# Kernel optimization log

Hardware: AMD Instinct MI355X
Metric: run time of the kernel (lower is better)

Reference implementation:

```python
import jax, jax.numpy as jnp
import numpy as np
from jax import lax

B, C, H, W = 32, 3, 128, 128
S = 10             # max_segments
L = 200            # base_traj_length
TOTAL_LIMIT = 200  # traj_length (must equal L per original sample())
DOF = 2
HID = 2048
CONV_OUT = 512 * 6 * 6  # 128->126->63->61->30->28->14->12->6


def _conv(x, w, b):
    y = lax.conv_general_dilated(x, w, (1, 1), 'VALID', dimension_numbers=('NCHW', 'OIHW', 'NCHW'))
    return y + b[None, :, None, None]


def _pool_relu(x):
    return jax.nn.relu(lax.reduce_window(x, -jnp.inf, lax.max, (1, 1, 2, 2), (1, 1, 2, 2), 'VALID'))


def _rotate2d(y, y0, rot):
    # rotate points y (B,L,2) around per-batch center y0 (B,2) by rot (B,1,1) radians
    px, py = y[..., 0:1], y[..., 1:2]
    cx, cy = y0[:, 0][:, None, None], y0[:, 1][:, None, None]
    c, s = jnp.cos(rot), jnp.sin(rot)
    return jnp.concatenate([c * (px - cx) - s * (py - cy) + cx,
                            s * (px - cx) + c * (py - cy) + cy], axis=2)


def _sample(traj, ratio):
    b, T = traj.shape[0], traj.shape[1]
    f32 = traj.dtype
    seg_limit = jnp.ceil(ratio * TOTAL_LIMIT)  # (B,S)
    # redistribution: shave 1 off the (first) max segment while over budget.
    # original runs over_limit.max() iterations; over_limit <= S-1, extras are no-ops (still_over gate).
    for _ in range(S):
        max_val = seg_limit.max(axis=1)
        still_over = (seg_limit.sum(axis=1) != float(L)).astype(f32)
        reduced = jnp.ones((b,), f32)
        for j in range(S):
            mult = jnp.abs(jnp.sign(max_val - seg_limit[:, j]) - 1.0)
            seg_limit = seg_limit.at[:, j].add(-mult * reduced * still_over)
            reduced = jnp.clip(reduced - mult, 0.0)
    seg_ids = np.arange(T) // L
    # replicates original condition: i>0 and cur_segment_idx != floor(i - 1/L)  (note: i - 1/L, as written)
    forces = np.array([(i > 0) and (seg_ids[i] != int(np.floor(i - 1.0 / L))) for i in range(T)])
    di0 = jnp.floor((L - 1.0) / seg_limit[:, 0:1])
    init = (di0, jnp.zeros((b, 1), f32), jnp.zeros((b, 1), f32), jnp.zeros((b, S), f32))

    def step(state, inp):
        di, last_idx, n_tot, seg_cnt = state
        i_f, seg, force = inp
        lim = lax.dynamic_index_in_dim(seg_limit, seg, axis=1, keepdims=True)  # (B,1)
        cnt = lax.dynamic_index_in_dim(seg_cnt, seg, axis=1, keepdims=True)    # (B,1)
        new_di = jnp.floor((L - 1.0 - (last_idx - seg.astype(f32) * L)) / (lim - cnt))
        di = jnp.where(force | (di < new_di), new_di, di)
        chk = (jnp.sign(jnp.clip(TOTAL_LIMIT - n_tot, 0.0))
               * (cnt < lim).astype(f32)
               * (i_f - last_idx == di).astype(f32))
        last_idx = jnp.maximum(last_idx, i_f * chk)
        seg_cnt = lax.dynamic_update_index_in_dim(seg_cnt, (cnt + chk)[:, 0], seg, axis=1)
        return (di, last_idx, n_tot + chk, seg_cnt), chk[:, 0]

    xs = (jnp.arange(T, dtype=f32), jnp.asarray(seg_ids, jnp.int32), jnp.asarray(forces))
    _, mask_t = lax.scan(step, init, xs)
    mask = mask_t.T > 0  # (B,T) velocity mask; exactly TOTAL_LIMIT true per row
    idx = jnp.argsort(jnp.where(mask, 0, 1), axis=1)[:, :TOTAL_LIMIT]  # stable sort -> ordered true positions
    return jnp.take_along_axis(traj, idx[:, :, None], axis=1)


def _forward(x, w1, b1, w2, b2, w3, b3, w4, b4, fcw1, fcb1, fcw2, fcb2,
             wi, bi, ws, bs, wr, br, base_traj):
    h = _pool_relu(_conv(x, w1, b1))
    h = _pool_relu(_conv(h, w2, b2))
    h = _pool_relu(_conv(h, w3, b3))
    h = _pool_relu(_conv(h, w4, b4))
    feat = h.reshape(h.shape[0], -1)  # (B, CONV_OUT)
    z = jnp.tanh(feat @ fcw1.T + fcb1)
    z = z @ fcw2.T + fcb2             # dropout == identity (eval mode)
    init_pos = z @ wi.T + bi                                   # (B,DOF)
    seg_mod = (z @ ws.T + bs).reshape(z.shape[0], S, DOF + 1)  # (B,S,DOF+1)
    ratio = jax.nn.softmax(z @ wr.T + br, axis=1)              # (B,S)
    last_pos = init_pos[:, None, :]
    starts, segs = [last_pos], []
    for i in range(S):
        scaling = seg_mod[:, i, :-1]
        rot = jnp.tanh(seg_mod[:, i, -1])[:, None, None] * 3.14
        m = base_traj * scaling[:, None, :]
        m = _rotate2d(m, m[:, 0, :], rot)
        m = last_pos + m
        last_pos = m[:, -1:, :]
        starts.append(last_pos)
        segs.append(m)
    traj = jnp.concatenate(segs, axis=1)             # (B,S*L,DOF) unsampled
    seg_start_end = jnp.concatenate(starts, axis=1)  # (B,S+1,DOF)
    sampled = _sample(traj, ratio)                   # (B,TOTAL_LIMIT,DOF)
    return sampled, seg_start_end, ratio, traj


def setup_inputs():
    key = jax.random.key(0)
    ks = jax.random.split(key, 12)
    n = lambda k, s, sc: jax.random.normal(k, s, jnp.float32) * sc
    t = jnp.linspace(0.0, 1.0, L)
    base_traj = jnp.stack([t, jnp.sin(t * jnp.pi)], axis=-1)[None]  # (1,L,2)
    return {
        'x': n(ks[0], (B, C, H, W), 1.0),
        'w1': n(ks[1], (64, C, 3, 3), 0.05), 'b1': jnp.zeros((64,), jnp.float32),
        'w2': n(ks[2], (128, 64, 3, 3), 0.05), 'b2': jnp.zeros((128,), jnp.float32),
        'w3': n(ks[3], (256, 128, 3, 3), 0.05), 'b3': jnp.zeros((256,), jnp.float32),
        'w4': n(ks[4], (512, 256, 3, 3), 0.05), 'b4': jnp.zeros((512,), jnp.float32),
        'fcw1': n(ks[5], (HID, CONV_OUT), 0.01), 'fcb1': jnp.zeros((HID,), jnp.float32),
        'fcw2': n(ks[6], (HID, HID), 0.02), 'fcb2': jnp.zeros((HID,), jnp.float32),
        'wi': n(ks[7], (DOF, HID), 0.02), 'bi': jnp.zeros((DOF,), jnp.float32),
        'ws': n(ks[8], (S * (DOF + 1), HID), 0.02), 'bs': jnp.zeros((S * (DOF + 1),), jnp.float32),
        'wr': n(ks[9], (S, HID), 0.05), 'br': jnp.zeros((S,), jnp.float32),
        'base_traj': base_traj,
    }


def reference(x, w1, b1, w2, b2, w3, b3, w4, b4, fcw1, fcb1, fcw2, fcb2,
              wi, bi, ws, bs, wr, br, base_traj):
    return _forward(x, w1, b1, w2, b2, w3, b3, w4, b4, fcw1, fcb1, fcw2, fcb2,
                    wi, bi, ws, bs, wr, br, base_traj)
```

## Files before the change

### kernel.cpp

```cpp
#include <hip/hip_runtime.h>

__global__ __launch_bounds__(256)
void conv1_lds(const float* __restrict__ in, const float* __restrict__ wt,
               const float* __restrict__ bias, float* __restrict__ out)
{
    __shared__ float sh[3][34][34];
    int bx = blockIdx.x;
    int tile = bx & 15;
    int cg   = (bx >> 4) & 7;
    int b    = bx >> 7;
    int tr = tile >> 2, tc = tile & 3;
    int tid = threadIdx.x;
    int ty = tid >> 4, tx = tid & 15;
    int R0 = 32 * tr, C0 = 32 * tc;

    for (int t = tid; t < 3 * 34 * 34; t += 256) {
        int ci = t / 1156;
        int rem = t - ci * 1156;
        int rr = rem / 34, cc = rem - rr * 34;
        int gr = R0 + rr; if (gr > 127) gr = 127;
        int gc = C0 + cc; if (gc > 127) gc = 127;
        sh[ci][rr][cc] = in[(((size_t)b * 3 + ci) * 128 + gr) * 128 + gc];
    }
    __syncthreads();

    float acc[8][2][2] = {};
    int co0 = cg * 8;
#pragma unroll
    for (int ci = 0; ci < 3; ++ci) {
        float p[4][4];
#pragma unroll
        for (int r = 0; r < 4; ++r) {
            const float2* pr = reinterpret_cast<const float2*>(&sh[ci][2 * ty + r][2 * tx]);
            float2 a = pr[0], c2 = pr[1];
            p[r][0] = a.x; p[r][1] = a.y; p[r][2] = c2.x; p[r][3] = c2.y;
        }
#pragma unroll
        for (int j = 0; j < 8; ++j) {
            const float* wj = wt + ((size_t)(co0 + j) * 3 + ci) * 9;
#pragma unroll
            for (int kh = 0; kh < 3; ++kh)
#pragma unroll
                for (int kw = 0; kw < 3; ++kw) {
                    float wv = wj[kh * 3 + kw];
#pragma unroll
                    for (int dy = 0; dy < 2; ++dy)
#pragma unroll
                        for (int dx = 0; dx < 2; ++dx)
                            acc[j][dy][dx] = fmaf(wv, p[dy + kh][dx + kw], acc[j][dy][dx]);
                }
        }
    }
    int py = 16 * tr + ty, px = 16 * tc + tx;
    if (py < 63 && px < 63) {
#pragma unroll
        for (int j = 0; j < 8; ++j) {
            float v = fmaxf(fmaxf(acc[j][0][0], acc[j][0][1]),
                            fmaxf(acc[j][1][0], acc[j][1][1])) + bias[co0 + j];
            out[(((size_t)b * 64 + co0 + j) * 63 + py) * 63 + px] = fmaxf(v, 0.f);
        }
    }
}

__global__ __launch_bounds__(256)
void conv2_db(const float* __restrict__ in, const float* __restrict__ wt,
              const float* __restrict__ bias, float* __restrict__ out)
{
    __shared__ __align__(16) float sh[4][32][34];

    int bx = blockIdx.x;
    int tile = bx & 3;
    int cg   = (bx >> 2) & 15;
    int b    = bx >> 6;
    int thi = tile >> 1, twi = tile & 1;
    int R0 = 30 * thi, C0 = 30 * twi;

    int tid = threadIdx.x;
    int ty = tid / 15, tx = tid - ty * 15;
    bool active = (tid < 225);
    int co0 = cg * 8;

    float acc[8][2][2] = {};
    float sr[16];

#pragma unroll
    for (int j = 0; j < 16; ++j) {
        int t = tid + 256 * j;
        int ci = t >> 10;
        int rem = t & 1023;
        int rr = rem >> 5, cc = rem & 31;
        sr[j] = in[(((size_t)b * 64 + ci) * 63 + (R0 + rr)) * 63 + (C0 + cc)];
    }

    for (int it = 0; it < 16; ++it) {
#pragma unroll
        for (int j = 0; j < 16; ++j) {
            int t = tid + 256 * j;
            int ci = t >> 10;
            int rem = t & 1023;
            int rr = rem >> 5, cc = rem & 31;
            sh[ci][rr][cc] = sr[j];
        }
        __syncthreads();
        if (it < 15) {
            int ci0n = (it + 1) * 4;
#pragma unroll
            for (int j = 0; j < 16; ++j) {
                int t = tid + 256 * j;
                int ci = t >> 10;
                int rem = t & 1023;
                int rr = rem >> 5, cc = rem & 31;
                sr[j] = in[(((size_t)b * 64 + ci0n + ci) * 63 + (R0 + rr)) * 63 + (C0 + cc)];
            }
        }
        if (active) {
            int ci0 = it * 4;
#pragma unroll
            for (int ci = 0; ci < 4; ++ci) {
                float p[4][4];
#pragma unroll
                for (int r = 0; r < 4; ++r) {
                    const float2* pr = reinterpret_cast<const float2*>(&sh[ci][2 * ty + r][2 * tx]);
                    float2 a = pr[0], c2 = pr[1];
                    p[r][0] = a.x; p[r][1] = a.y; p[r][2] = c2.x; p[r][3] = c2.y;
                }
#pragma unroll
                for (int j = 0; j < 8; ++j) {
                    const float* wj = wt + ((size_t)(co0 + j) * 64 + (ci0 + ci)) * 9;
#pragma unroll
                    for (int kh = 0; kh < 3; ++kh)
#pragma unroll
                        for (int kw = 0; kw < 3; ++kw) {
                            float wv = wj[kh * 3 + kw];
#pragma unroll
                            for (int dy = 0; dy < 2; ++dy)
#pragma unroll
                                for (int dx = 0; dx < 2; ++dx)
                                    acc[j][dy][dx] = fmaf(wv, p[dy + kh][dx + kw], acc[j][dy][dx]);
                        }
                }
            }
        }
        __syncthreads();
    }
    if (active) {
        int py = 15 * thi + ty, px = 15 * twi + tx;
#pragma unroll
        for (int j = 0; j < 8; ++j) {
            float v = fmaxf(fmaxf(acc[j][0][0], acc[j][0][1]),
                            fmaxf(acc[j][1][0], acc[j][1][1])) + bias[co0 + j];
            out[(((size_t)b * 128 + co0 + j) * 30 + py) * 30 + px] = fmaxf(v, 0.f);
        }
    }
}

__global__ __launch_bounds__(256)
void conv3_db(const float* __restrict__ in, const float* __restrict__ wt,
              const float* __restrict__ bias, float* __restrict__ out)
{
    __shared__ float4 sh4[900];
    float* shf = reinterpret_cast<float*>(sh4);

    int bx = blockIdx.x;
    int cg = bx & 31;
    int b  = bx >> 5;
    int tid = threadIdx.x;
    int ty = tid / 14, tx = tid - ty * 14;
    bool active = (tid < 196);
    int co0 = cg * 8;

    float acc[8][2][2] = {};
    float4 sr[4];

    const float4* gp0 = reinterpret_cast<const float4*>(in + (size_t)b * 128 * 900);
#pragma unroll
    for (int j = 0; j < 4; ++j) {
        int idx = tid + 256 * j;
        if (idx < 900) sr[j] = gp0[idx];
    }

    for (int it = 0; it < 32; ++it) {
#pragma unroll
        for (int j = 0; j < 4; ++j) {
            int idx = tid + 256 * j;
            if (idx < 900) sh4[idx] = sr[j];
        }
        __syncthreads();
        if (it < 31) {
            const float4* gpn = gp0 + (size_t)(it + 1) * 900;
#pragma unroll
            for (int j = 0; j < 4; ++j) {
                int idx = tid + 256 * j;
                if (idx < 900) sr[j] = gpn[idx];
            }
        }
        if (active) {
            int ci0 = it * 4;
#pragma unroll
            for (int ci = 0; ci < 4; ++ci) {
                const float* base = shf + ci * 900;
                float p[4][4];
#pragma unroll
                for (int r = 0; r < 4; ++r) {
                    const float2* pr = reinterpret_cast<const float2*>(base + (2 * ty + r) * 30 + 2 * tx);
                    float2 a = pr[0], c2 = pr[1];
                    p[r][0] = a.x; p[r][1] = a.y; p[r][2] = c2.x; p[r][3] = c2.y;
                }
#pragma unroll
                for (int j = 0; j < 8; ++j) {
                    const float* wj = wt + ((size_t)(co0 + j) * 128 + (ci0 + ci)) * 9;
#pragma unroll
                    for (int kh = 0; kh < 3; ++kh)
#pragma unroll
                        for (int kw = 0; kw < 3; ++kw) {
                            float wv = wj[kh * 3 + kw];
#pragma unroll
                            for (int dy = 0; dy < 2; ++dy)
#pragma unroll
                                for (int dx = 0; dx < 2; ++dx)
                                    acc[j][dy][dx] = fmaf(wv, p[dy + kh][dx + kw], acc[j][dy][dx]);
                        }
                }
            }
        }
        __syncthreads();
    }
    if (active) {
#pragma unroll
        for (int j = 0; j < 8; ++j) {
            float v = fmaxf(fmaxf(acc[j][0][0], acc[j][0][1]),
                            fmaxf(acc[j][1][0], acc[j][1][1])) + bias[co0 + j];
            out[(((size_t)b * 256 + co0 + j) * 14 + ty) * 14 + tx] = fmaxf(v, 0.f);
        }
    }
}

__global__ __launch_bounds__(256)
void conv4_v3(const float* __restrict__ in, const float* __restrict__ wt,
              const float* __restrict__ bias, float* __restrict__ out)
{
    __shared__ __align__(16) float smem[4032 + 4 * 16 * 37];
    float* in_sh = smem;
    float* w_sh  = smem + 4032;
    float* red   = smem;

    int bx = blockIdx.x;
    int cg = bx & 31;
    int b  = bx >> 5;
    int tid = threadIdx.x;
    int h   = tid >> 6;
    int r6  = tid & 63;
    int cog = r6 >> 3;
    int sub = r6 & 7;
    int R = 3 * (sub >> 1), C = 6 * (sub & 1);

    float acc[2][3][6] = {};
    float sin_r[13];
    float sw_r[9];

    const size_t in_b = (size_t)b * 256 * 196;

#pragma unroll
    for (int j = 0; j < 13; ++j) {
        int g = tid + 256 * j;
        if (g < 3136) {
            int hh = g / 784, rem = g - hh * 784;
            int ci = rem / 196, r2 = rem - ci * 196;
            sin_r[j] = in[in_b + (size_t)(hh * 64 + ci) * 196 + r2];
        }
    }
#pragma unroll
    for (int j = 0; j < 9; ++j) {
        int g = tid + 256 * j;
        int hh = g / 576, rem = g - hh * 576;
        int co = rem / 36, q = rem - co * 36;
        sw_r[j] = wt[(size_t)(cg * 16 + co) * 2304 + (size_t)(hh * 64) * 9 + q];
    }

    for (int it = 0; it < 16; ++it) {
#pragma unroll
        for (int j = 0; j < 13; ++j) {
            int g = tid + 256 * j;
            if (g < 3136) {
                int hh = g / 784, rem = g - hh * 784;
                int ci = rem / 196, r2 = rem - ci * 196;
                int rr = r2 / 14, cc = r2 - rr * 14;
                in_sh[((hh * 4 + ci) * 14 + rr) * 18 + cc] = sin_r[j];
            }
        }
#pragma unroll
        for (int j = 0; j < 9; ++j) {
            int g = tid + 256 * j;
            int hh = g / 576, rem = g - hh * 576;
            int co = rem / 36, q = rem - co * 36;
            w_sh[(hh * 16 + co) * 37 + q] = sw_r[j];
        }
        __syncthreads();
        if (it < 15) {
            int k0n = (it + 1) * 4;
#pragma unroll
            for (int j = 0; j < 13; ++j) {
                int g = tid + 256 * j;
                if (g < 3136) {
                    int hh = g / 784, rem = g - hh * 784;
                    int ci = rem / 196, r2 = rem - ci * 196;
                    sin_r[j] = in[in_b + (size_t)(hh * 64 + k0n + ci) * 196 + r2];
                }
            }
#pragma unroll
            for (int j = 0; j < 9; ++j) {
                int g = tid + 256 * j;
                int hh = g / 576, rem = g - hh * 576;
                int co = rem / 36, q = rem - co * 36;
                sw_r[j] = wt[(size_t)(cg * 16 + co) * 2304 + (size_t)(hh * 64 + k0n) * 9 + q];
            }
        }
#pragma unroll
        for (int ci = 0; ci < 4; ++ci) {
            float w[2][9];
#pragma unroll
            for (int c = 0; c < 2; ++c)
#pragma unroll
                for (int k = 0; k < 9; ++k)
                    w[c][k] = w_sh[(h * 16 + 2 * cog + c) * 37 + ci * 9 + k];
            const float* rowbase = in_sh + ((h * 4 + ci) * 14) * 18;
#pragma unroll
            for (int r = 0; r < 5; ++r) {
                float row[8];
                const float2* pr = reinterpret_cast<const float2*>(rowbase + (size_t)(R + r) * 18 + C);
                float2 a0 = pr[0], a1 = pr[1], a2 = pr[2], a3 = pr[3];
                row[0] = a0.x; row[1] = a0.y; row[2] = a1.x; row[3] = a1.y;
                row[4] = a2.x; row[5] = a2.y; row[6] = a3.x; row[7] = a3.y;
#pragma unroll
                for (int y = 0; y < 3; ++y) {
                    if (y < r - 2 || y > r) continue;
                    int kh = r - y;
#pragma unroll
                    for (int c = 0; c < 2; ++c)
#pragma unroll
                        for (int kw = 0; kw < 3; ++kw) {
                            float wv = w[c][kh * 3 + kw];
#pragma unroll
                            for (int x = 0; x < 6; ++x)
                                acc[c][y][x] = fmaf(wv, row[x + kw], acc[c][y][x]);
                        }
                }
            }
        }
        __syncthreads();
    }
#pragma unroll
    for (int hh = 0; hh < 4; ++hh) {
        if (h == hh) {
#pragma unroll
            for (int c = 0; c < 2; ++c)
#pragma unroll
                for (int y = 0; y < 3; ++y)
#pragma unroll
                    for (int x = 0; x < 6; ++x) {
                        float* dst = &red[((2 * cog + c) * 12 + R + y) * 13 + C + x];
                        if (hh == 0) *dst = acc[c][y][x];
                        else         *dst += acc[c][y][x];
                    }
        }
        __syncthreads();
    }
    for (int t = tid; t < 576; t += 256) {
        int co = t / 36, rem = t - co * 36;
        int pr = rem / 6, pc = rem - pr * 6;
        const float* rp = &red[(co * 12 + 2 * pr) * 13 + 2 * pc];
        float v = fmaxf(fmaxf(rp[0], rp[1]), fmaxf(rp[13], rp[14]));
        v += bias[cg * 16 + co];
        out[(((size_t)b * 512 + cg * 16 + co) * 6 + pr) * 6 + pc] = fmaxf(v, 0.f);
    }
}

__global__ __launch_bounds__(1024)
void fc_big(const float* __restrict__ X, const float* __restrict__ W,
            const float* __restrict__ bias, float* __restrict__ Y,
            int K, int N, int act)
{
    __shared__ float red[32][32][8];
    int o0 = blockIdx.x * 8;
    int s = threadIdx.x & 31;
    int b = threadIdx.x >> 5;
    int K4 = K >> 2;
    const float4* X4 = reinterpret_cast<const float4*>(X) + (size_t)b * K4;
    const float4* W4 = reinterpret_cast<const float4*>(W);

    float acc[8] = {};
    for (int k4 = s; k4 < K4; k4 += 32) {
        float4 xv = X4[k4];
#pragma unroll
        for (int o = 0; o < 8; ++o) {
            float4 wv = W4[(size_t)(o0 + o) * K4 + k4];
            acc[o] = fmaf(xv.x, wv.x,
                     fmaf(xv.y, wv.y,
                     fmaf(xv.z, wv.z,
                     fmaf(xv.w, wv.w, acc[o]))));
        }
    }
#pragma unroll
    for (int o = 0; o < 8; ++o) red[b][s][o] = acc[o];
    __syncthreads();
    if (threadIdx.x < 256) {
        int bb = threadIdx.x >> 3, oo = threadIdx.x & 7;
        float v = bias[o0 + oo];
#pragma unroll 8
        for (int ss = 0; ss < 32; ++ss) v += red[bb][ss][oo];
        if (act) v = tanhf(v);
        Y[(size_t)bb * N + o0 + oo] = v;
    }
}

__global__ __launch_bounds__(256)
void fc_two(const float* __restrict__ X, const float* __restrict__ W,
            const float* __restrict__ bias, float* __restrict__ Y,
            int K, int N, int act)
{
    int o0 = blockIdx.x * 2;
    int tid = threadIdx.x;
    const float* w0 = W + (size_t)o0 * K;
    const float* w1 = w0 + K;
    float a0[32], a1[32];
#pragma unroll
    for (int b = 0; b < 32; ++b) { a0[b] = 0.f; a1[b] = 0.f; }

    for (int k = tid; k < K; k += 256) {
        float wv0 = w0[k], wv1 = w1[k];
#pragma unroll
        for (int b = 0; b < 32; ++b) {
            float xv = X[(size_t)b * K + k];
            a0[b] = fmaf(wv0, xv, a0[b]);
            a1[b] = fmaf(wv1, xv, a1[b]);
        }
    }
    __shared__ float part[2][4][32];
    int lane = tid & 63, wv = tid >> 6;
#pragma unroll
    for (int b = 0; b < 32; ++b) {
        float s0 = a0[b], s1 = a1[b];
#pragma unroll
        for (int off = 32; off >= 1; off >>= 1) {
            s0 += __shfl_down(s0, off);
            s1 += __shfl_down(s1, off);
        }
        if (lane == 0) { part[0][wv][b] = s0; part[1][wv][b] = s1; }
    }
    __syncthreads();
    if (tid < 64) {
        int j = tid >> 5, b = tid & 31;
        float s = part[j][0][b] + part[j][1][b] + part[j][2][b] + part[j][3][b] + bias[o0 + j];
        if (act) s = tanhf(s);
        Y[(size_t)b * N + o0 + j] = s;
    }
}

__global__ __launch_bounds__(64)
void post_kernel(const float* __restrict__ logits, float* __restrict__ ratio_out,
                 float* __restrict__ sl_out)
{
    int b = threadIdx.x;
    if (b >= 32) return;
    float lg[10];
#pragma unroll
    for (int j = 0; j < 10; ++j) lg[j] = logits[b * 10 + j];
    float mx = lg[0];
#pragma unroll
    for (int j = 1; j < 10; ++j) mx = fmaxf(mx, lg[j]);
    float e[10]; float ssum = 0.f;
#pragma unroll
    for (int j = 0; j < 10; ++j) { e[j] = expf(lg[j] - mx); ssum += e[j]; }
    float sl[10];
#pragma unroll
    for (int j = 0; j < 10; ++j) {
        float r = e[j] / ssum;
        ratio_out[b * 10 + j] = r;
        sl[j] = ceilf(r * 200.f);
    }
#pragma unroll
    for (int it = 0; it < 10; ++it) {
        float s = 0.f, mx2 = sl[0];
#pragma unroll
        for (int j = 0; j < 10; ++j) { s += sl[j]; mx2 = fmaxf(mx2, sl[j]); }
        float over = (s != 200.f) ? 1.f : 0.f;
        float reduced = 1.f;
#pragma unroll
        for (int j = 0; j < 10; ++j) {
            float mult = (sl[j] == mx2) ? 1.f : 0.f;
            sl[j] -= mult * reduced * over;
            reduced = fmaxf(reduced - mult, 0.f);
        }
    }
#pragma unroll
    for (int j = 0; j < 10; ++j) sl_out[b * 10 + j] = sl[j];
}

__global__ __launch_bounds__(256)
void traj_kernel(const float* __restrict__ base, const float* __restrict__ ipos,
                 const float* __restrict__ sm, float* __restrict__ out_traj,
                 float* __restrict__ out_starts)
{
    int b = blockIdx.x;
    int j = threadIdx.x;
    float bx0 = base[0], by0 = base[1];
    float bxL = base[398], byL = base[399];
    float bx = 0.f, by = 0.f;
    if (j < 200) { bx = base[2 * j]; by = base[2 * j + 1]; }
    float curx = ipos[b * 2 + 0], cury = ipos[b * 2 + 1];
    if (j == 0) { out_starts[b * 22 + 0] = curx; out_starts[b * 22 + 1] = cury; }
#pragma unroll
    for (int i = 0; i < 10; ++i) {
        float sx  = sm[b * 30 + i * 3 + 0];
        float sy  = sm[b * 30 + i * 3 + 1];
        float rot = tanhf(sm[b * 30 + i * 3 + 2]) * 3.14f;
        float c = cosf(rot), s = sinf(rot);
        float cx = bx0 * sx, cy = by0 * sy;
        if (j < 200) {
            float px = bx * sx, py = by * sy;
            float rx = c * (px - cx) - s * (py - cy) + cx;
            float ry = s * (px - cx) + c * (py - cy) + cy;
            size_t o = ((size_t)b * 2000 + i * 200 + j) * 2;
            out_traj[o + 0] = curx + rx;
            out_traj[o + 1] = cury + ry;
        }
        float pxL = bxL * sx, pyL = byL * sy;
        float exL = c * (pxL - cx) - s * (pyL - cy) + cx;
        float eyL = s * (pxL - cx) + c * (pyL - cy) + cy;
        curx += exL; cury += eyL;
        if (j == 0) {
            out_starts[b * 22 + (i + 1) * 2 + 0] = curx;
            out_starts[b * 22 + (i + 1) * 2 + 1] = cury;
        }
    }
}

__global__ __launch_bounds__(64)
void sample_kernel(const float* __restrict__ sl_in, const float* __restrict__ traj,
                   float* __restrict__ samp_out)
{
    __shared__ unsigned int maskb[32][63];
    __shared__ float ssl[32][10];
    int tid = threadIdx.x;
    for (int t = tid; t < 32 * 63; t += 64) ((unsigned int*)maskb)[t] = 0u;
    for (int t = tid; t < 32 * 10; t += 64) ((float*)ssl)[t] = sl_in[t];
    __syncthreads();
    if (tid >= 32) return;
    int b = tid;
    const float* tb = traj + (size_t)b * 4000;
    float* sp = samp_out + (size_t)b * 400;
    int out_n = 0;
    float last = 0.f, ntot = 0.f;
    float lim0 = ssl[b][0];
    float di = floorf(199.f / lim0);
    float ct0 = 0.f;
    if ((ntot < 200.f) && (ct0 < lim0) && (0.f - last == di)) {
        ntot += 1.f; ct0 += 1.f;
        maskb[b][0] |= 1u;
        sp[out_n * 2] = tb[0]; sp[out_n * 2 + 1] = tb[1]; ++out_n;
    }
    {
        float ndi = floorf((199.f - last) / (lim0 - ct0));
        if (di < ndi) di = ndi;
        if ((ntot < 200.f) && (ct0 < lim0) && (1.f - last == di)) {
            last = 1.f; ntot += 1.f; ct0 += 1.f;
            maskb[b][0] |= 2u;
            sp[out_n * 2] = tb[2]; sp[out_n * 2 + 1] = tb[3]; ++out_n;
        }
    }
    for (int seg = 0; seg < 10; ++seg) {
        float lim = ssl[b][seg];
        float ct = (seg == 0) ? ct0 : 0.f;
        float segbase = 200.f * seg;
        float segend = segbase + 199.f;
        float pos = (seg == 0) ? 2.f : segbase;
        float ndi = floorf((199.f - (last - segbase)) / (lim - ct));
        while ((ntot < 200.f) && (ct < lim)) {
            float fi = last + ndi;
            if (!(fi >= pos && fi <= segend)) break;
            int i = (int)fi;
            last = fi; ntot += 1.f; ct += 1.f;
            maskb[b][i >> 5] |= (1u << (i & 31));
            sp[out_n * 2] = tb[2 * i]; sp[out_n * 2 + 1] = tb[2 * i + 1]; ++out_n;
            pos = fi + 1.f;
            ndi = floorf((199.f - (last - segbase)) / (lim - ct));
        }
    }
    for (int i = 0; i < 2000 && out_n < 200; ++i) {
        if (!((maskb[b][i >> 5] >> (i & 31)) & 1u)) {
            sp[out_n * 2] = tb[2 * i]; sp[out_n * 2 + 1] = tb[2 * i + 1]; ++out_n;
        }
    }
}

extern "C" void kernel_launch(void* const* d_in, const int* in_sizes, int n_in,
                              void* d_out, int out_size, void* d_ws, size_t ws_size,
                              hipStream_t stream)
{
    const float* x    = (const float*)d_in[0];
    const float* w1   = (const float*)d_in[1];
    const float* b1   = (const float*)d_in[2];
    const float* w2   = (const float*)d_in[3];
    const float* b2   = (const float*)d_in[4];
    const float* w3   = (const float*)d_in[5];
    const float* b3   = (const float*)d_in[6];
    const float* w4   = (const float*)d_in[7];
    const float* b4   = (const float*)d_in[8];
    const float* fcw1 = (const float*)d_in[9];
    const float* fcb1 = (const float*)d_in[10];
    const float* fcw2 = (const float*)d_in[11];
    const float* fcb2 = (const float*)d_in[12];
    const float* wi   = (const float*)d_in[13];
    const float* bi   = (const float*)d_in[14];
    const float* wsw  = (const float*)d_in[15];
    const float* bs   = (const float*)d_in[16];
    const float* wr   = (const float*)d_in[17];
    const float* br   = (const float*)d_in[18];
    const float* base = (const float*)d_in[19];

    float* out = (float*)d_out;
    float* ws  = (float*)d_ws;

    float* p1   = ws + 0;
    float* p2   = ws + 8128512;
    float* p3   = ws + 0;
    float* feat = ws + 8128512;
    float* z1   = ws + 0;
    float* z2   = ws + 65536;
    float* ipos = ws + 131072;
    float* smod = ws + 131136;
    float* rlog = ws + 132096;
    float* slim = ws + 132416;

    float* out_samp   = out;
    float* out_starts = out + 12800;
    float* out_ratio  = out + 13504;
    float* out_traj   = out + 13824;

    conv1_lds<<<4096, 256, 0, stream>>>(x, w1, b1, p1);
    conv2_db<<<2048, 256, 0, stream>>>(p1, w2, b2, p2);
    conv3_db<<<1024, 256, 0, stream>>>(p2, w3, b3, p3);
    conv4_v3<<<1024, 256, 0, stream>>>(p3, w4, b4, feat);

    fc_big<<<256, 1024, 0, stream>>>(feat, fcw1, fcb1, z1, 18432, 2048, 1);
    fc_big<<<256, 1024, 0, stream>>>(z1, fcw2, fcb2, z2, 2048, 2048, 0);

    fc_two<<<1, 256, 0, stream>>>(z2, wi, bi, ipos, 2048, 2, 0);
    fc_two<<<15, 256, 0, stream>>>(z2, wsw, bs, smod, 2048, 30, 0);
    fc_two<<<5, 256, 0, stream>>>(z2, wr, br, rlog, 2048, 10, 0);

    post_kernel<<<1, 64, 0, stream>>>(rlog, out_ratio, slim);
    traj_kernel<<<32, 256, 0, stream>>>(base, ipos, smod, out_traj, out_starts);
    sample_kernel<<<1, 64, 0, stream>>>(slim, out_traj, out_samp);
}
```

Baseline: 994.9 us.

## Double-buffer LDS in conv2/conv3 and widen conv2 to 16 output channels

Conv2 and conv3 now keep two shared-memory input buffers, so each iteration needs one barrier instead of two, and the next chunk is written to the spare buffer after compute. Conv2 also computes 16 output channels per block instead of 8, which halves the grid and the redundant input tile loads per channel. The cost is more registers (64 accumulators in conv2) and twice the shared memory, which may reduce occupancy.

Measured after the change: 1.206 ms. 21.3% more time.

```diff
diff --git a/kernel.cpp b/kernel.cpp
--- a/kernel.cpp
+++ b/kernel.cpp
@@ -63,24 +63,24 @@
 }
 
 __global__ __launch_bounds__(256)
-void conv2_db(const float* __restrict__ in, const float* __restrict__ wt,
+void conv2_v3(const float* __restrict__ in, const float* __restrict__ wt,
               const float* __restrict__ bias, float* __restrict__ out)
 {
-    __shared__ __align__(16) float sh[4][32][34];
+    __shared__ __align__(16) float sh[2][4][32][34];
 
     int bx = blockIdx.x;
     int tile = bx & 3;
-    int cg   = (bx >> 2) & 15;
-    int b    = bx >> 6;
+    int cg   = (bx >> 2) & 7;
+    int b    = bx >> 5;
     int thi = tile >> 1, twi = tile & 1;
     int R0 = 30 * thi, C0 = 30 * twi;
 
     int tid = threadIdx.x;
     int ty = tid / 15, tx = tid - ty * 15;
     bool active = (tid < 225);
-    int co0 = cg * 8;
-
-    float acc[8][2][2] = {};
+    int co0 = cg * 16;
+
+    float acc[16][2][2] = {};
     float sr[16];
 
 #pragma unroll
@@ -91,17 +91,18 @@
         int rr = rem >> 5, cc = rem & 31;
         sr[j] = in[(((size_t)b * 64 + ci) * 63 + (R0 + rr)) * 63 + (C0 + cc)];
     }
+#pragma unroll
+    for (int j = 0; j < 16; ++j) {
+        int t = tid + 256 * j;
+        int ci = t >> 10;
+        int rem = t & 1023;
+        int rr = rem >> 5, cc = rem & 31;
+        sh[0][ci][rr][cc] = sr[j];
+    }
+    __syncthreads();
 
     for (int it = 0; it < 16; ++it) {
-#pragma unroll
-        for (int j = 0; j < 16; ++j) {
-            int t = tid + 256 * j;
-            int ci = t >> 10;
-            int rem = t & 1023;
-            int rr = rem >> 5, cc = rem & 31;
-            sh[ci][rr][cc] = sr[j];
-        }
-        __syncthreads();
+        int cur = it & 1;
         if (it < 15) {
             int ci0n = (it + 1) * 4;
 #pragma unroll
@@ -114,19 +115,18 @@
             }
         }
         if (active) {
-            int ci0 = it * 4;
 #pragma unroll
             for (int ci = 0; ci < 4; ++ci) {
                 float p[4][4];
 #pragma unroll
                 for (int r = 0; r < 4; ++r) {
-                    const float2* pr = reinterpret_cast<const float2*>(&sh[ci][2 * ty + r][2 * tx]);
+                    const float2* pr = reinterpret_cast<const float2*>(&sh[cur][ci][2 * ty + r][2 * tx]);
                     float2 a = pr[0], c2 = pr[1];
                     p[r][0] = a.x; p[r][1] = a.y; p[r][2] = c2.x; p[r][3] = c2.y;
                 }
 #pragma unroll
-                for (int j = 0; j < 8; ++j) {
-                    const float* wj = wt + ((size_t)(co0 + j) * 64 + (ci0 + ci)) * 9;
+                for (int j = 0; j < 16; ++j) {
+                    const float* wj = wt + ((size_t)(co0 + j) * 64 + (it * 4 + ci)) * 9;
 #pragma unroll
                     for (int kh = 0; kh < 3; ++kh)
 #pragma unroll
@@ -141,12 +141,22 @@
                 }
             }
         }
+        if (it < 15) {
+#pragma unroll
+            for (int j = 0; j < 16; ++j) {
+                int t = tid + 256 * j;
+                int ci = t >> 10;
+                int rem = t & 1023;
+                int rr = rem >> 5, cc = rem & 31;
+                sh[cur ^ 1][ci][rr][cc] = sr[j];
+            }
+        }
         __syncthreads();
     }
     if (active) {
         int py = 15 * thi + ty, px = 15 * twi + tx;
 #pragma unroll
-        for (int j = 0; j < 8; ++j) {
+        for (int j = 0; j < 16; ++j) {
             float v = fmaxf(fmaxf(acc[j][0][0], acc[j][0][1]),
                             fmaxf(acc[j][1][0], acc[j][1][1])) + bias[co0 + j];
             out[(((size_t)b * 128 + co0 + j) * 30 + py) * 30 + px] = fmaxf(v, 0.f);
@@ -158,8 +168,7 @@
 void conv3_db(const float* __restrict__ in, const float* __restrict__ wt,
               const float* __restrict__ bias, float* __restrict__ out)
 {
-    __shared__ float4 sh4[900];
-    float* shf = reinterpret_cast<float*>(sh4);
+    __shared__ float4 sh4[2][900];
 
     int bx = blockIdx.x;
     int cg = bx & 31;
@@ -178,14 +187,15 @@
         int idx = tid + 256 * j;
         if (idx < 900) sr[j] = gp0[idx];
     }
+#pragma unroll
+    for (int j = 0; j < 4; ++j) {
+        int idx = tid + 256 * j;
+        if (idx < 900) sh4[0][idx] = sr[j];
+    }
+    __syncthreads();
 
     for (int it = 0; it < 32; ++it) {
-#pragma unroll
-        for (int j = 0; j < 4; ++j) {
-            int idx = tid + 256 * j;
-            if (idx < 900) sh4[idx] = sr[j];
-        }
-        __syncthreads();
+        int cur = it & 1;
         if (it < 31) {
             const float4* gpn = gp0 + (size_t)(it + 1) * 900;
 #pragma unroll
@@ -195,7 +205,7 @@
             }
         }
         if (active) {
-            int ci0 = it * 4;
+            const float* shf = reinterpret_cast<const float*>(sh4[cur]);
 #pragma unroll
             for (int ci = 0; ci < 4; ++ci) {
                 const float* base = shf + ci * 900;
@@ -208,7 +218,7 @@
                 }
 #pragma unroll
                 for (int j = 0; j < 8; ++j) {
-                    const float* wj = wt + ((size_t)(co0 + j) * 128 + (ci0 + ci)) * 9;
+                    const float* wj = wt + ((size_t)(co0 + j) * 128 + (it * 4 + ci)) * 9;
 #pragma unroll
                     for (int kh = 0; kh < 3; ++kh)
 #pragma unroll
@@ -221,6 +231,13 @@
                                     acc[j][dy][dx] = fmaf(wv, p[dy + kh][dx + kw], acc[j][dy][dx]);
                         }
                 }
+            }
+        }
+        if (it < 31) {
+#pragma unroll
+            for (int j = 0; j < 4; ++j) {
+                int idx = tid + 256 * j;
+                if (idx < 900) sh4[cur ^ 1][idx] = sr[j];
             }
         }
         __syncthreads();
@@ -638,7 +655,7 @@
     float* out_traj   = out + 13824;
 
     conv1_lds<<<4096, 256, 0, stream>>>(x, w1, b1, p1);
-    conv2_db<<<2048, 256, 0, stream>>>(p1, w2, b2, p2);
+    conv2_v3<<<1024, 256, 0, stream>>>(p1, w2, b2, p2);
     conv3_db<<<1024, 256, 0, stream>>>(p2, w3, b3, p3);
     conv4_v3<<<1024, 256, 0, stream>>>(p3, w4, b4, feat);
 
```

## Replace conv2/conv3 with templated register-tiled conv using per-thread channel and 4x8 outputs

Applied to the files above, without the earlier changes.

Conv2 and conv3 are replaced by a single templated kernel. Each thread owns one output channel and a 4x8 pre-pool output patch. Weights are loaded once per input channel into registers and reused across 32 outputs, and the input rows are read from LDS once per row. The old kernels had each thread handle 8 channels and a 2x2 patch, which reloaded weights for every channel and re-read the input. The new layout raises arithmetic intensity and also fixes the thread mapping so all 256 threads do work. The cost is more registers and edge tiles that do wasted compute.

Result: no change. 995.5 us (+0.1%).

```diff
diff --git a/kernel.cpp b/kernel.cpp
--- a/kernel.cpp
+++ b/kernel.cpp
@@ -62,175 +62,115 @@
     }
 }
 
+template<int CIN, int DIM, int POOL, int COUT, int TILES_R, int TILES_C>
 __global__ __launch_bounds__(256)
-void conv2_db(const float* __restrict__ in, const float* __restrict__ wt,
-              const float* __restrict__ bias, float* __restrict__ out)
-{
-    __shared__ __align__(16) float sh[4][32][34];
+void conv_v4(const float* __restrict__ in, const float* __restrict__ wt,
+             const float* __restrict__ bias, float* __restrict__ out)
+{
+    __shared__ __align__(16) float sh[4][18][34];
 
     int bx = blockIdx.x;
-    int tile = bx & 3;
-    int cg   = (bx >> 2) & 15;
-    int b    = bx >> 6;
-    int thi = tile >> 1, twi = tile & 1;
-    int R0 = 30 * thi, C0 = 30 * twi;
-
+    constexpr int NT = TILES_R * TILES_C;
+    constexpr int NCG = COUT / 16;
+    int tile = bx % NT;
+    int cg   = (bx / NT) % NCG;
+    int b    = bx / (NT * NCG);
+    int rt = tile / TILES_C, ct = tile % TILES_C;
     int tid = threadIdx.x;
-    int ty = tid / 15, tx = tid - ty * 15;
-    bool active = (tid < 225);
-    int co0 = cg * 8;
-
-    float acc[8][2][2] = {};
-    float sr[16];
-
-#pragma unroll
-    for (int j = 0; j < 16; ++j) {
+    int co_l = tid & 15;
+    int sp   = tid >> 4;
+    int ty = sp >> 2, tx = sp & 3;
+    int co = cg * 16 + co_l;
+
+    int R0 = 16 * rt, C0 = 32 * ct;
+
+    float acc[4][8] = {};
+    float sr[10];
+
+    const size_t in_b = (size_t)b * CIN * DIM * DIM;
+    const float* wco = wt + (size_t)co * CIN * 9;
+
+#pragma unroll
+    for (int j = 0; j < 10; ++j) {
         int t = tid + 256 * j;
-        int ci = t >> 10;
-        int rem = t & 1023;
-        int rr = rem >> 5, cc = rem & 31;
-        sr[j] = in[(((size_t)b * 64 + ci) * 63 + (R0 + rr)) * 63 + (C0 + cc)];
-    }
-
-    for (int it = 0; it < 16; ++it) {
-#pragma unroll
-        for (int j = 0; j < 16; ++j) {
+        if (t < 2448) {
+            int ci = t / 612;
+            int rem = t - ci * 612;
+            int rr = rem / 34, cc = rem - rr * 34;
+            int gr = R0 + rr; if (gr > DIM - 1) gr = DIM - 1;
+            int gc = C0 + cc; if (gc > DIM - 1) gc = DIM - 1;
+            sr[j] = in[in_b + (size_t)ci * DIM * DIM + gr * DIM + gc];
+        }
+    }
+
+    constexpr int ITERS = CIN / 4;
+    for (int it = 0; it < ITERS; ++it) {
+#pragma unroll
+        for (int j = 0; j < 10; ++j) {
             int t = tid + 256 * j;
-            int ci = t >> 10;
-            int rem = t & 1023;
-            int rr = rem >> 5, cc = rem & 31;
-            sh[ci][rr][cc] = sr[j];
+            if (t < 2448) {
+                int ci = t / 612;
+                int rem = t - ci * 612;
+                int rr = rem / 34, cc = rem - rr * 34;
+                sh[ci][rr][cc] = sr[j];
+            }
         }
         __syncthreads();
-        if (it < 15) {
+        if (it < ITERS - 1) {
             int ci0n = (it + 1) * 4;
 #pragma unroll
-            for (int j = 0; j < 16; ++j) {
+            for (int j = 0; j < 10; ++j) {
                 int t = tid + 256 * j;
-                int ci = t >> 10;
-                int rem = t & 1023;
-                int rr = rem >> 5, cc = rem & 31;
-                sr[j] = in[(((size_t)b * 64 + ci0n + ci) * 63 + (R0 + rr)) * 63 + (C0 + cc)];
-            }
-        }
-        if (active) {
-            int ci0 = it * 4;
-#pragma unroll
-            for (int ci = 0; ci < 4; ++ci) {
-                float p[4][4];
-#pragma unroll
-                for (int r = 0; r < 4; ++r) {
-                    const float2* pr = reinterpret_cast<const float2*>(&sh[ci][2 * ty + r][2 * tx]);
-                    float2 a = pr[0], c2 = pr[1];
-                    p[r][0] = a.x; p[r][1] = a.y; p[r][2] = c2.x; p[r][3] = c2.y;
+                if (t < 2448) {
+                    int ci = t / 612;
+                    int rem = t - ci * 612;
+                    int rr = rem / 34, cc = rem - rr * 34;
+                    int gr = R0 + rr; if (gr > DIM - 1) gr = DIM - 1;
+                    int gc = C0 + cc; if (gc > DIM - 1) gc = DIM - 1;
+                    sr[j] = in[in_b + (size_t)(ci0n + ci) * DIM * DIM + gr * DIM + gc];
                 }
-#pragma unroll
-                for (int j = 0; j < 8; ++j) {
-                    const float* wj = wt + ((size_t)(co0 + j) * 64 + (ci0 + ci)) * 9;
-#pragma unroll
-                    for (int kh = 0; kh < 3; ++kh)
-#pragma unroll
-                        for (int kw = 0; kw < 3; ++kw) {
-                            float wv = wj[kh * 3 + kw];
-#pragma unroll
-                            for (int dy = 0; dy < 2; ++dy)
-#pragma unroll
-                                for (int dx = 0; dx < 2; ++dx)
-                                    acc[j][dy][dx] = fmaf(wv, p[dy + kh][dx + kw], acc[j][dy][dx]);
-                        }
+            }
+        }
+#pragma unroll
+        for (int ci = 0; ci < 4; ++ci) {
+            float w[9];
+#pragma unroll
+            for (int k = 0; k < 9; ++k) w[k] = wco[(it * 4 + ci) * 9 + k];
+#pragma unroll
+            for (int r = 0; r < 6; ++r) {
+                float row[10];
+                const float2* pr = reinterpret_cast<const float2*>(&sh[ci][4 * ty + r][8 * tx]);
+                float2 v0 = pr[0], v1 = pr[1], v2 = pr[2], v3 = pr[3], v4 = pr[4];
+                row[0] = v0.x; row[1] = v0.y; row[2] = v1.x; row[3] = v1.y; row[4] = v2.x;
+                row[5] = v2.y; row[6] = v3.x; row[7] = v3.y; row[8] = v4.x; row[9] = v4.y;
+#pragma unroll
+                for (int y = 0; y < 4; ++y) {
+                    if (y < r - 2 || y > r) continue;
+                    int kh = r - y;
+#pragma unroll
+                    for (int kw = 0; kw < 3; ++kw) {
+                        float wv = w[kh * 3 + kw];
+#pragma unroll
+                        for (int x = 0; x < 8; ++x)
+                            acc[y][x] = fmaf(wv, row[x + kw], acc[y][x]);
+                    }
                 }
             }
         }
         __syncthreads();
     }
-    if (active) {
-        int py = 15 * thi + ty, px = 15 * twi + tx;
-#pragma unroll
-        for (int j = 0; j < 8; ++j) {
-            float v = fmaxf(fmaxf(acc[j][0][0], acc[j][0][1]),
-                            fmaxf(acc[j][1][0], acc[j][1][1])) + bias[co0 + j];
-            out[(((size_t)b * 128 + co0 + j) * 30 + py) * 30 + px] = fmaxf(v, 0.f);
-        }
-    }
-}
-
-__global__ __launch_bounds__(256)
-void conv3_db(const float* __restrict__ in, const float* __restrict__ wt,
-              const float* __restrict__ bias, float* __restrict__ out)
-{
-    __shared__ float4 sh4[900];
-    float* shf = reinterpret_cast<float*>(sh4);
-
-    int bx = blockIdx.x;
-    int cg = bx & 31;
-    int b  = bx >> 5;
-    int tid = threadIdx.x;
-    int ty = tid / 14, tx = tid - ty * 14;
-    bool active = (tid < 196);
-    int co0 = cg * 8;
-
-    float acc[8][2][2] = {};
-    float4 sr[4];
-
-    const float4* gp0 = reinterpret_cast<const float4*>(in + (size_t)b * 128 * 900);
-#pragma unroll
-    for (int j = 0; j < 4; ++j) {
-        int idx = tid + 256 * j;
-        if (idx < 900) sr[j] = gp0[idx];
-    }
-
-    for (int it = 0; it < 32; ++it) {
-#pragma unroll
-        for (int j = 0; j < 4; ++j) {
-            int idx = tid + 256 * j;
-            if (idx < 900) sh4[idx] = sr[j];
-        }
-        __syncthreads();
-        if (it < 31) {
-            const float4* gpn = gp0 + (size_t)(it + 1) * 900;
-#pragma unroll
-            for (int j = 0; j < 4; ++j) {
-                int idx = tid + 256 * j;
-                if (idx < 900) sr[j] = gpn[idx];
-            }
-        }
-        if (active) {
-            int ci0 = it * 4;
-#pragma unroll
-            for (int ci = 0; ci < 4; ++ci) {
-                const float* base = shf + ci * 900;
-                float p[4][4];
-#pragma unroll
-                for (int r = 0; r < 4; ++r) {
-                    const float2* pr = reinterpret_cast<const float2*>(base + (2 * ty + r) * 30 + 2 * tx);
-                    float2 a = pr[0], c2 = pr[1];
-                    p[r][0] = a.x; p[r][1] = a.y; p[r][2] = c2.x; p[r][3] = c2.y;
-                }
-#pragma unroll
-                for (int j = 0; j < 8; ++j) {
-                    const float* wj = wt + ((size_t)(co0 + j) * 128 + (ci0 + ci)) * 9;
-#pragma unroll
-                    for (int kh = 0; kh < 3; ++kh)
-#pragma unroll
-                        for (int kw = 0; kw < 3; ++kw) {
-                            float wv = wj[kh * 3 + kw];
-#pragma unroll
-                            for (int dy = 0; dy < 2; ++dy)
-#pragma unroll
-                                for (int dx = 0; dx < 2; ++dx)
-                                    acc[j][dy][dx] = fmaf(wv, p[dy + kh][dx + kw], acc[j][dy][dx]);
-                        }
-                }
-            }
-        }
-        __syncthreads();
-    }
-    if (active) {
-#pragma unroll
-        for (int j = 0; j < 8; ++j) {
-            float v = fmaxf(fmaxf(acc[j][0][0], acc[j][0][1]),
-                            fmaxf(acc[j][1][0], acc[j][1][1])) + bias[co0 + j];
-            out[(((size_t)b * 256 + co0 + j) * 14 + ty) * 14 + tx] = fmaxf(v, 0.f);
+    float bz = bias[co];
+#pragma unroll
+    for (int dy = 0; dy < 2; ++dy) {
+        int py = 8 * rt + 2 * ty + dy;
+#pragma unroll
+        for (int dx = 0; dx < 4; ++dx) {
+            int px = 16 * ct + 4 * tx + dx;
+            if (py < POOL && px < POOL) {
+                float v = fmaxf(fmaxf(acc[2 * dy][2 * dx],     acc[2 * dy][2 * dx + 1]),
+                                fmaxf(acc[2 * dy + 1][2 * dx], acc[2 * dy + 1][2 * dx + 1]));
+                out[(((size_t)b * COUT + co) * POOL + py) * POOL + px] = fmaxf(v + bz, 0.f);
+            }
         }
     }
 }
@@ -638,8 +578,8 @@
     float* out_traj   = out + 13824;
 
     conv1_lds<<<4096, 256, 0, stream>>>(x, w1, b1, p1);
-    conv2_db<<<2048, 256, 0, stream>>>(p1, w2, b2, p2);
-    conv3_db<<<1024, 256, 0, stream>>>(p2, w3, b3, p3);
+    conv_v4<64, 63, 30, 128, 4, 2><<<2048, 256, 0, stream>>>(p1, w2, b2, p2);
+    conv_v4<128, 30, 14, 256, 2, 1><<<1024, 256, 0, stream>>>(p2, w3, b3, p3);
     conv4_v3<<<1024, 256, 0, stream>>>(p3, w4, b4, feat);
 
     fc_big<<<256, 1024, 0, stream>>>(feat, fcw1, fcb1, z1, 18432, 2048, 1);
```
